# Performance work log

Measured on AMD Instinct MI355X. Metric: run time of the kernel, lower is better.

Reference implementation:

```python
import jax, jax.numpy as jnp
import numpy as np

NUMSTEPS = 10  # message-passing rounds (SeqGGNN numsteps)

def setup_inputs() -> dict:
    key = jax.random.key(0)
    ks = jax.random.split(key, 10)
    B, S, H, V = 64, 512, 256, 32000
    s = 0.05  # keep activations in a stable range
    return {
        "x": jax.random.randint(ks[0], (B, S), 0, V),
        "emb": jax.random.normal(ks[1], (V, H), jnp.float32) * s,
        "W_edge": jax.random.normal(ks[2], (3, H, H), jnp.float32) * s,  # [fwd, bwd, self]
        "b_edge": jax.random.normal(ks[3], (3, H), jnp.float32) * s,
        "W_ih": jax.random.normal(ks[4], (3 * H, H), jnp.float32) * s,
        "W_hh": jax.random.normal(ks[5], (3 * H, H), jnp.float32) * s,
        "b_ih": jax.random.normal(ks[6], (3 * H,), jnp.float32) * s,
        "b_hh": jax.random.normal(ks[7], (3 * H,), jnp.float32) * s,
        "out_w": jax.random.normal(ks[8], (V, H), jnp.float32) * s,
        "out_b": jax.random.normal(ks[9], (V,), jnp.float32) * s,
    }

def _gru(m, h, W_ih, W_hh, b_ih, b_hh):
    # torch.nn.GRUCell semantics with input m, state h
    gi = m @ W_ih.T + b_ih
    gh = h @ W_hh.T + b_hh
    i_r, i_z, i_n = jnp.split(gi, 3, axis=-1)
    h_r, h_z, h_n = jnp.split(gh, 3, axis=-1)
    r = jax.nn.sigmoid(i_r + h_r)
    z = jax.nn.sigmoid(i_z + h_z)
    n = jnp.tanh(i_n + r * h_n)
    return (1.0 - z) * n + z * h

def reference(x, emb, W_edge, b_edge, W_ih, W_hh, b_ih, b_hh, out_w, out_b):
    # x: [B,S] int ids; chain graph per row with 3 edge types:
    #   fwd:  j -> j+1 (node j+1 receives W_edge[0] h_j + b_edge[0])
    #   bwd:  j+1 -> j (node j receives W_edge[1] h_{j+1} + b_edge[1])
    #   self: j -> j   (W_edge[2] h_j + b_edge[2])
    h0 = emb[x]  # [B,S,H]

    def step(h, _):
        t_fwd = jnp.einsum('bsh,hk->bsk', h, W_edge[0]) + b_edge[0]
        t_bwd = jnp.einsum('bsh,hk->bsk', h, W_edge[1]) + b_edge[1]
        m_self = jnp.einsum('bsh,hk->bsk', h, W_edge[2]) + b_edge[2]
        # scatter-sum along the chain == shift with zero pad at boundaries
        m_fwd = jnp.pad(t_fwd[:, :-1], ((0, 0), (1, 0), (0, 0)))
        m_bwd = jnp.pad(t_bwd[:, 1:], ((0, 0), (0, 1), (0, 0)))
        m = m_fwd + m_bwd + m_self
        h_new = _gru(m, h, W_ih, W_hh, b_ih, b_hh)
        return h_new, None

    h, _ = jax.lax.scan(step, h0, None, length=NUMSTEPS)
    last = h[:, -1, :]  # [B,H]
    return last @ out_w.T + out_b  # [B,V]
```

## Files before the change

kernel.cpp:

```cpp
#include <hip/hip_runtime.h>
#include <math.h>

#define Bb 64
#define Ss 512
#define Hh 256
#define Vv 32000
#define BS (Bb*Ss)
#define NSTEPS 10

typedef __attribute__((ext_vector_type(8))) short bf16x8;
typedef __attribute__((ext_vector_type(4))) float f32x4;
typedef unsigned short u16;

#define MFMA(a,b,c) __builtin_amdgcn_mfma_f32_16x16x32_bf16((a),(b),(c),0,0,0)

__device__ __forceinline__ u16 f2bf(float f) {
    unsigned u = __float_as_uint(f);
    u += 0x7fffu + ((u >> 16) & 1u);
    return (u16)(u >> 16);
}
__device__ __forceinline__ float bf2f(u16 h) {
    return __uint_as_float(((unsigned)h) << 16);
}
__device__ __forceinline__ int nmap(int j, int g) {
    return ((j >> 4) << 6) | (g << 4) | (j & 15);
}
#define GLL(src, dst) __builtin_amdgcn_global_load_lds( \
    (const __attribute__((address_space(1))) void*)(src), \
    (__attribute__((address_space(3))) void*)(dst), 16, 0, 0)

__global__ __launch_bounds__(256)
void k_prep_big(const float* __restrict__ We, const float* __restrict__ Wih,
                const float* __restrict__ Whh, u16* __restrict__ Bbig) {
    __shared__ u16 Aps[64 * 32];
    __shared__ u16 Bps[64 * 32];
    const int p = blockIdx.y, seg = p / 3, g = p % 3;
    const int segmap0 = (seg == 0) ? 2 : (seg == 1 ? 0 : 1);
    const float* Wseg = We + segmap0 * 65536;
    const int kt = (blockIdx.x >> 2) * 64, jt = (blockIdx.x & 3) * 64;
    const int t = threadIdx.x;
    const int lane = t & 63, wid = t >> 6;
    const int wy = (wid >> 1) * 32, wx = (wid & 1) * 32;
    const int lr = lane & 15, hi = lane >> 4;

    f32x4 acc[2][2];
    #pragma unroll
    for (int a = 0; a < 2; ++a)
        #pragma unroll
        for (int b = 0; b < 2; ++b) acc[a][b] = 0.0f;

    for (int ks = 0; ks < 8; ++ks) {
        const int k0 = ks * 32;
        {
            int r = t >> 2, kc = t & 3;
            const float* sa = Wseg + (kt + r) * 256 + k0 + kc * 8;
            float4 a0 = *(const float4*)sa, a1 = *(const float4*)(sa + 4);
            bf16x8 va;
            va[0]=(short)f2bf(a0.x); va[1]=(short)f2bf(a0.y); va[2]=(short)f2bf(a0.z); va[3]=(short)f2bf(a0.w);
            va[4]=(short)f2bf(a1.x); va[5]=(short)f2bf(a1.y); va[6]=(short)f2bf(a1.z); va[7]=(short)f2bf(a1.w);
            ((bf16x8*)Aps)[r * 4 + (kc ^ (r & 3))] = va;
            const float* sb = Wih + (g * 256 + jt + r) * 256 + k0 + kc * 8;
            float4 b0 = *(const float4*)sb, b1 = *(const float4*)(sb + 4);
            bf16x8 vb;
            vb[0]=(short)f2bf(b0.x); vb[1]=(short)f2bf(b0.y); vb[2]=(short)f2bf(b0.z); vb[3]=(short)f2bf(b0.w);
            vb[4]=(short)f2bf(b1.x); vb[5]=(short)f2bf(b1.y); vb[6]=(short)f2bf(b1.z); vb[7]=(short)f2bf(b1.w);
            ((bf16x8*)Bps)[r * 4 + (kc ^ (r & 3))] = vb;
        }
        __syncthreads();
        bf16x8 af[2], bfv[2];
        #pragma unroll
        for (int f = 0; f < 2; ++f) {
            int ra = wy + f * 16 + lr;
            af[f]  = ((const bf16x8*)Aps)[ra * 4 + (hi ^ (ra & 3))];
            int rb = wx + f * 16 + lr;
            bfv[f] = ((const bf16x8*)Bps)[rb * 4 + (hi ^ (rb & 3))];
        }
        #pragma unroll
        for (int fm = 0; fm < 2; ++fm)
            #pragma unroll
            for (int fn = 0; fn < 2; ++fn)
                acc[fm][fn] = MFMA(af[fm], bfv[fn], acc[fm][fn]);
        __syncthreads();
    }
    #pragma unroll
    for (int fm = 0; fm < 2; ++fm)
        #pragma unroll
        for (int fn = 0; fn < 2; ++fn) {
            int kbase = kt + wy + fm * 16 + hi * 4;
            int j     = jt + wx + fn * 16 + lr;
            float4 wv = make_float4(0.f, 0.f, 0.f, 0.f);
            if (seg == 0 && g < 2)
                wv = *(const float4*)(Whh + (g * 256 + j) * 256 + kbase);
            ushort4 o;
            o.x = f2bf(acc[fm][fn][0] + wv.x);
            o.y = f2bf(acc[fm][fn][1] + wv.y);
            o.z = f2bf(acc[fm][fn][2] + wv.z);
            o.w = f2bf(acc[fm][fn][3] + wv.w);
            *(ushort4*)(Bbig + (size_t)nmap(j, g) * 768 + seg * 256 + kbase) = o;
        }
}

__global__ __launch_bounds__(256)
void k_prep_hn(const float* __restrict__ Whh, u16* __restrict__ Bbig) {
    int j = blockIdx.x / 3;
    int k = (blockIdx.x % 3) * 256 + threadIdx.x;
    Bbig[(size_t)nmap(j, 3) * 768 + k] =
        (k < 256) ? f2bf(Whh[(512 + j) * 256 + k]) : (u16)0;
}

__global__ __launch_bounds__(256)
void k_prep_bias(const float* __restrict__ Wih, const float* __restrict__ b_edge,
                 const float* __restrict__ b_ih, const float* __restrict__ b_hh,
                 float* __restrict__ bias) {
    int id = blockIdx.x * 256 + threadIdx.x;
    int c = id >> 10, n = id & 1023;
    int g = (n >> 4) & 3;
    int j = ((n >> 6) << 4) | (n & 15);
    float a;
    if (g == 3) {
        a = b_hh[512 + j];
    } else {
        a = b_ih[g * 256 + j] + (g < 2 ? b_hh[g * 256 + j] : 0.f);
        const float* wrow = Wih + (g * 256 + j) * 256;
        for (int k = 0; k < 256; ++k) {
            float eb = b_edge[512 + k] + (c != 0 ? b_edge[k] : 0.f)
                     + (c != 2 ? b_edge[256 + k] : 0.f);
            a += eb * wrow[k];
        }
    }
    bias[c * 1024 + n] = a;
}

__global__ __launch_bounds__(256)
void k_prep_zp(u16* __restrict__ zp) {
    zp[blockIdx.x * 256 + threadIdx.x] = 0;
}

__global__ __launch_bounds__(256)
void k_embed(const int* __restrict__ x, const float* __restrict__ emb,
             u16* __restrict__ h) {
    int idx = blockIdx.x * 256 + threadIdx.x;
    int row = idx >> 5, c8 = idx & 31;
    long long tok = x[row];
    const float4* e = reinterpret_cast<const float4*>(emb + tok * Hh + c8 * 8);
    float4 a = e[0], b = e[1];
    bf16x8 v;
    v[0]=(short)f2bf(a.x); v[1]=(short)f2bf(a.y); v[2]=(short)f2bf(a.z); v[3]=(short)f2bf(a.w);
    v[4]=(short)f2bf(b.x); v[5]=(short)f2bf(b.y); v[6]=(short)f2bf(b.z); v[7]=(short)f2bf(b.w);
    ((bf16x8*)h)[idx] = v;
}

__global__ __launch_bounds__(512, 2)
void k_step(const u16* __restrict__ hin, const u16* __restrict__ Bbig,
            const float* __restrict__ bias, const u16* __restrict__ zp,
            u16* __restrict__ hout) {
    __shared__ __attribute__((aligned(16))) u16 As[2][2][128 * 64];
    __shared__ __attribute__((aligned(16))) u16 Bs[2][2][128 * 64];
    const int t = threadIdx.x;
    const int lane = t & 63, wid = t >> 6;
    const int swz = (blockIdx.x & 7) * 64 + (blockIdx.x >> 3);
    const int rowBlk = (swz >> 2) * 256;
    const int colBlk = (swz & 3) * 256;
    const int wy = wid >> 2, wx = wid & 3;
    const int lr = lane & 15, hi = lane >> 4;
    const int s0 = rowBlk & (Ss - 1);

    const int q   = t >> 3;
    const int off = ((t & 7) ^ (q & 7)) << 3;
    const int xo  = lr & 7;

    const u16* pB[4];
    #pragma unroll
    for (int j = 0; j < 4; ++j)
        pB[j] = Bbig + (size_t)(colBlk + j * 64 + q) * 768 + off;

    f32x4 acc[8][4];
    #pragma unroll
    for (int a = 0; a < 8; ++a)
        #pragma unroll
        for (int b = 0; b < 4; ++b) acc[a][b] = 0.0f;

    #pragma unroll
    for (int h = 0; h < 2; ++h)
        #pragma unroll
        for (int i = 0; i < 2; ++i) {
            int rh = h * 128 + i * 64 + q;
            GLL(hin + (size_t)(rowBlk + rh) * Hh + off,
                &As[0][h][(i * 512 + wid * 64) * 8]);
            GLL(pB[h * 2 + i], &Bs[0][h][(i * 512 + wid * 64) * 8]);
        }
    #pragma unroll
    for (int j = 0; j < 4; ++j) pB[j] += 64;
    __syncthreads();

    #pragma unroll
    for (int seg = 0; seg < 3; ++seg) {
        #pragma unroll
        for (int t4 = 0; t4 < 4; ++t4) {
            const int tt = seg * 4 + t4;
            const int b  = tt & 1, nb = b ^ 1;
            const int tn = tt + 1;
            const int segn = tn >> 2;
            const int dn   = (segn == 0) ? 0 : (segn == 1 ? -1 : 1);
            const int k0n  = (tn & 3) * 64;
            #pragma unroll
            for (int kk = 0; kk < 2; ++kk) {
                bf16x8 bf[4];
                #pragma unroll
                for (int mh = 0; mh < 2; ++mh) {
                    if (tt < 11 && kk == 0) {
                        if (mh == 0) {
                            #pragma unroll
                            for (int h = 0; h < 2; ++h)
                                #pragma unroll
                                for (int i = 0; i < 2; ++i) {
                                    int rh = h * 128 + i * 64 + q;
                                    int ss = s0 + rh + dn;
                                    const u16* src = (ss >= 0 && ss < Ss)
                                        ? hin + (size_t)(rowBlk + rh + dn) * Hh + k0n + off
                                        : zp;
                                    GLL(src, &As[nb][h][(i * 512 + wid * 64) * 8]);
                                }
                        } else {
                            #pragma unroll
                            for (int h = 0; h < 2; ++h)
                                #pragma unroll
                                for (int i = 0; i < 2; ++i)
                                    GLL(pB[h * 2 + i], &Bs[nb][h][(i * 512 + wid * 64) * 8]);
                            #pragma unroll
                            for (int j = 0; j < 4; ++j) pB[j] += 64;
                        }
                    }
                    if (mh == 0) {
                        #pragma unroll
                        for (int f = 0; f < 4; ++f) {
                            if (seg != 0 && f == 3) continue;
                            int rwb = (wx & 1) * 64 + f * 16 + lr;
                            bf[f] = ((const bf16x8*)Bs[b][wx >> 1])
                                        [rwb * 8 + ((kk * 4 + hi) ^ xo)];
                        }
                    }
                    bf16x8 af[4];
                    #pragma unroll
                    for (int f = 0; f < 4; ++f) {
                        int rwa = mh * 64 + f * 16 + lr;
                        af[f] = ((const bf16x8*)As[b][wy])
                                    [rwa * 8 + ((kk * 4 + hi) ^ xo)];
                    }
                    __builtin_amdgcn_s_setprio(1);
                    #pragma unroll
                    for (int fm = 0; fm < 4; ++fm)
                        #pragma unroll
                        for (int fn = 0; fn < 4; ++fn)
                            if (seg == 0 || fn < 3)
                                acc[mh * 4 + fm][fn] =
                                    MFMA(af[fm], bf[fn], acc[mh * 4 + fm][fn]);
                    __builtin_amdgcn_s_setprio(0);
                }
            }
            __syncthreads();
        }
    }

    const int hq = (colBlk >> 2) + wx * 16;
    #pragma unroll
    for (int mf = 0; mf < 8; ++mf)
        #pragma unroll
        for (int i = 0; i < 4; ++i) {
            int row = rowBlk + wy * 128 + mf * 16 + hi * 4 + i;
            int s = row & (Ss - 1);
            int cls = (s == 0) ? 0 : ((s == Ss - 1) ? 2 : 1);
            const float* bp = bias + cls * 1024 + colBlk + wx * 64 + lr;
            float vr = acc[mf][0][i] + bp[0];
            float vz = acc[mf][1][i] + bp[16];
            float vn = acc[mf][2][i] + bp[32];
            float vh = acc[mf][3][i] + bp[48];
            float r = 1.f / (1.f + __expf(-vr));
            float z = 1.f / (1.f + __expf(-vz));
            float e = __expf(2.f * (vn + r * vh));
            float n = 1.f - 2.f / (e + 1.f);
            int hcol = hq + lr;
            float hold = bf2f(hin[(size_t)row * Hh + hcol]);
            hout[(size_t)row * Hh + hcol] = f2bf(n + z * (hold - n));
        }
}

__global__ __launch_bounds__(256)
void k_out(const u16* __restrict__ h, const float* __restrict__ out_w,
           const float* __restrict__ out_b, float* __restrict__ out) {
    __shared__ u16 As[64 * 256];
    const int t = threadIdx.x;
    const int lane = t & 63, wid = t >> 6;
    const int colBlk = blockIdx.x * 128;
    const int wc = wid * 32;
    const int lr = lane & 15, hi = lane >> 4;

    #pragma unroll
    for (int i = 0; i < 8; ++i) {
        int c = t + i * 256;
        int r = c >> 5, kc = c & 31;
        bf16x8 v = *(const bf16x8*)(h + ((size_t)(r * Ss + (Ss - 1))) * Hh + kc * 8);
        ((bf16x8*)As)[r * 32 + (kc ^ (r & 7))] = v;
    }
    __syncthreads();

    f32x4 acc[4][2];
    #pragma unroll
    for (int a = 0; a < 4; ++a) { acc[a][0] = 0.0f; acc[a][1] = 0.0f; }

    #pragma unroll
    for (int ks = 0; ks < 8; ++ks) {
        bf16x8 af[4];
        #pragma unroll
        for (int f = 0; f < 4; ++f) {
            int ra = f * 16 + lr;
            af[f] = ((const bf16x8*)As)[ra * 32 + ((ks * 4 + hi) ^ (ra & 7))];
        }
        #pragma unroll
        for (int fn = 0; fn < 2; ++fn) {
            int n = colBlk + wc + fn * 16 + lr;
            const float* wp = out_w + (size_t)n * 256 + ks * 32 + hi * 8;
            float4 w0 = *(const float4*)wp, w1 = *(const float4*)(wp + 4);
            bf16x8 vb;
            vb[0]=(short)f2bf(w0.x); vb[1]=(short)f2bf(w0.y); vb[2]=(short)f2bf(w0.z); vb[3]=(short)f2bf(w0.w);
            vb[4]=(short)f2bf(w1.x); vb[5]=(short)f2bf(w1.y); vb[6]=(short)f2bf(w1.z); vb[7]=(short)f2bf(w1.w);
            #pragma unroll
            for (int fm = 0; fm < 4; ++fm)
                acc[fm][fn] = MFMA(af[fm], vb, acc[fm][fn]);
        }
    }
    #pragma unroll
    for (int fm = 0; fm < 4; ++fm)
        #pragma unroll
        for (int fn = 0; fn < 2; ++fn)
            #pragma unroll
            for (int i = 0; i < 4; ++i) {
                int row = fm * 16 + hi * 4 + i;
                int col = colBlk + wc + fn * 16 + lr;
                out[(size_t)row * Vv + col] = acc[fm][fn][i] + out_b[col];
            }
}

extern "C" void kernel_launch(void* const* d_in, const int* in_sizes, int n_in,
                              void* d_out, int out_size, void* d_ws, size_t ws_size,
                              hipStream_t stream) {
    const int*   x      = (const int*)  d_in[0];
    const float* emb    = (const float*)d_in[1];
    const float* W_edge = (const float*)d_in[2];
    const float* b_edge = (const float*)d_in[3];
    const float* W_ih   = (const float*)d_in[4];
    const float* W_hh   = (const float*)d_in[5];
    const float* b_ih   = (const float*)d_in[6];
    const float* b_hh   = (const float*)d_in[7];
    const float* out_w  = (const float*)d_in[8];
    const float* out_b  = (const float*)d_in[9];
    float* out = (float*)d_out;

    u16* hA   = (u16*)d_ws;
    u16* hB   = hA + (size_t)BS * Hh;
    u16* Bbig = hB + (size_t)BS * Hh;
    float* bias = (float*)(Bbig + (size_t)1024 * 768);
    u16* zp   = (u16*)(bias + 3 * 1024);

    k_prep_big <<<dim3(16, 9), 256, 0, stream>>>(W_edge, W_ih, W_hh, Bbig);
    k_prep_hn  <<<768, 256, 0, stream>>>(W_hh, Bbig);
    k_prep_bias<<<12, 256, 0, stream>>>(W_ih, b_edge, b_ih, b_hh, bias);
    k_prep_zp  <<<2, 256, 0, stream>>>(zp);
    k_embed    <<<BS * Hh / 8 / 256, 256, 0, stream>>>(x, emb, hA);

    u16* cur = hA;
    u16* nxt = hB;
    for (int step = 0; step < NSTEPS; ++step) {
        k_step<<<512, 512, 0, stream>>>(cur, Bbig, bias, zp, nxt);
        u16* tmp = cur; cur = nxt; nxt = tmp;
    }
    k_out<<<Vv / 128, 256, 0, stream>>>(cur, out_w, out_b, out);
}
```

Measured before the change: 571.2 us.

## Restructure step GEMM main loop into 4-stage K=32 pipeline with fine-grained waits

```diff
diff --git a/kernel.cpp b/kernel.cpp
--- a/kernel.cpp
+++ b/kernel.cpp
@@ -154,8 +154,8 @@
 void k_step(const u16* __restrict__ hin, const u16* __restrict__ Bbig,
             const float* __restrict__ bias, const u16* __restrict__ zp,
             u16* __restrict__ hout) {
-    __shared__ __attribute__((aligned(16))) u16 As[2][2][128 * 64];
-    __shared__ __attribute__((aligned(16))) u16 Bs[2][2][128 * 64];
+    __shared__ __attribute__((aligned(16))) u16 As[4][256 * 32];
+    __shared__ __attribute__((aligned(16))) u16 Bs[4][256 * 32];
     const int t = threadIdx.x;
     const int lane = t & 63, wid = t >> 6;
     const int swz = (blockIdx.x & 7) * 64 + (blockIdx.x >> 3);
@@ -165,14 +165,22 @@
     const int lr = lane & 15, hi = lane >> 4;
     const int s0 = rowBlk & (Ss - 1);
 
-    const int q   = t >> 3;
-    const int off = ((t & 7) ^ (q & 7)) << 3;
-    const int xo  = lr & 7;
-
-    const u16* pB[4];
-    #pragma unroll
-    for (int j = 0; j < 4; ++j)
-        pB[j] = Bbig + (size_t)(colBlk + j * 64 + q) * 768 + off;
+    const int q  = t >> 2;
+    const int kc = t & 3;
+    const u16* baseA[2];
+    const u16* baseB[2];
+    bool edgeLo[2], edgeHi[2];
+    u16* dstOff[2];
+    const u16* zpSafe = zp + 512;
+    #pragma unroll
+    for (int j = 0; j < 2; ++j) {
+        int r  = q + j * 128;
+        int ci = kc ^ (r & 3);
+        baseA[j] = hin  + (size_t)(rowBlk + r) * Hh  + ci * 8;
+        baseB[j] = Bbig + (size_t)(colBlk + r) * 768 + ci * 8;
+        edgeLo[j] = (s0 == 0   && r == 0);
+        edgeHi[j] = (s0 + r == 511);
+    }
 
     f32x4 acc[8][4];
     #pragma unroll
@@ -180,86 +188,61 @@
         #pragma unroll
         for (int b = 0; b < 4; ++b) acc[a][b] = 0.0f;
 
-    #pragma unroll
-    for (int h = 0; h < 2; ++h)
-        #pragma unroll
-        for (int i = 0; i < 2; ++i) {
-            int rh = h * 128 + i * 64 + q;
-            GLL(hin + (size_t)(rowBlk + rh) * Hh + off,
-                &As[0][h][(i * 512 + wid * 64) * 8]);
-            GLL(pB[h * 2 + i], &Bs[0][h][(i * 512 + wid * 64) * 8]);
-        }
-    #pragma unroll
-    for (int j = 0; j < 4; ++j) pB[j] += 64;
-    __syncthreads();
-
-    #pragma unroll
-    for (int seg = 0; seg < 3; ++seg) {
-        #pragma unroll
-        for (int t4 = 0; t4 < 4; ++t4) {
-            const int tt = seg * 4 + t4;
-            const int b  = tt & 1, nb = b ^ 1;
-            const int tn = tt + 1;
-            const int segn = tn >> 2;
-            const int dn   = (segn == 0) ? 0 : (segn == 1 ? -1 : 1);
-            const int k0n  = (tn & 3) * 64;
-            #pragma unroll
-            for (int kk = 0; kk < 2; ++kk) {
-                bf16x8 bf[4];
+    auto STAGE = [&](int tt) {
+        const int seg = tt >> 3;
+        const int d   = (seg == 0) ? 0 : (seg == 1 ? -1 : 1);
+        const int aOff = d * Hh + (tt & 7) * 32;
+        u16* aD = (u16*)As[tt & 3];
+        u16* bD = (u16*)Bs[tt & 3];
+        #pragma unroll
+        for (int j = 0; j < 2; ++j) {
+            const u16* sa = ((d < 0 && edgeLo[j]) || (d > 0 && edgeHi[j]))
+                          ? zpSafe : baseA[j];
+            GLL(sa + aOff,            aD + (size_t)(t + j * 512) * 8);
+            GLL(baseB[j] + tt * 32,   bD + (size_t)(t + j * 512) * 8);
+        }
+    };
+    auto COMPUTE = [&](int tt) {
+        const int seg = tt >> 3;
+        const bf16x8* aB = (const bf16x8*)As[tt & 3];
+        const bf16x8* bB = (const bf16x8*)Bs[tt & 3];
+        bf16x8 bf[4];
+        #pragma unroll
+        for (int f = 0; f < 4; ++f) {
+            if (seg != 0 && f == 3) continue;
+            int rb = wx * 64 + f * 16 + lr;
+            bf[f] = bB[rb * 4 + (hi ^ (rb & 3))];
+        }
+        #pragma unroll
+        for (int mh = 0; mh < 2; ++mh) {
+            bf16x8 af[4];
+            #pragma unroll
+            for (int f = 0; f < 4; ++f) {
+                int ra = wy * 128 + mh * 64 + f * 16 + lr;
+                af[f] = aB[ra * 4 + (hi ^ (ra & 3))];
+            }
+            __builtin_amdgcn_s_setprio(1);
+            #pragma unroll
+            for (int fm = 0; fm < 4; ++fm)
                 #pragma unroll
-                for (int mh = 0; mh < 2; ++mh) {
-                    if (tt < 11 && kk == 0) {
-                        if (mh == 0) {
-                            #pragma unroll
-                            for (int h = 0; h < 2; ++h)
-                                #pragma unroll
-                                for (int i = 0; i < 2; ++i) {
-                                    int rh = h * 128 + i * 64 + q;
-                                    int ss = s0 + rh + dn;
-                                    const u16* src = (ss >= 0 && ss < Ss)
-                                        ? hin + (size_t)(rowBlk + rh + dn) * Hh + k0n + off
-                                        : zp;
-                                    GLL(src, &As[nb][h][(i * 512 + wid * 64) * 8]);
-                                }
-                        } else {
-                            #pragma unroll
-                            for (int h = 0; h < 2; ++h)
-                                #pragma unroll
-                                for (int i = 0; i < 2; ++i)
-                                    GLL(pB[h * 2 + i], &Bs[nb][h][(i * 512 + wid * 64) * 8]);
-                            #pragma unroll
-                            for (int j = 0; j < 4; ++j) pB[j] += 64;
-                        }
-                    }
-                    if (mh == 0) {
-                        #pragma unroll
-                        for (int f = 0; f < 4; ++f) {
-                            if (seg != 0 && f == 3) continue;
-                            int rwb = (wx & 1) * 64 + f * 16 + lr;
-                            bf[f] = ((const bf16x8*)Bs[b][wx >> 1])
-                                        [rwb * 8 + ((kk * 4 + hi) ^ xo)];
-                        }
-                    }
-                    bf16x8 af[4];
-                    #pragma unroll
-                    for (int f = 0; f < 4; ++f) {
-                        int rwa = mh * 64 + f * 16 + lr;
-                        af[f] = ((const bf16x8*)As[b][wy])
-                                    [rwa * 8 + ((kk * 4 + hi) ^ xo)];
-                    }
-                    __builtin_amdgcn_s_setprio(1);
-                    #pragma unroll
-                    for (int fm = 0; fm < 4; ++fm)
-                        #pragma unroll
-                        for (int fn = 0; fn < 4; ++fn)
-                            if (seg == 0 || fn < 3)
-                                acc[mh * 4 + fm][fn] =
-                                    MFMA(af[fm], bf[fn], acc[mh * 4 + fm][fn]);
-                    __builtin_amdgcn_s_setprio(0);
-                }
-            }
-            __syncthreads();
-        }
+                for (int fn = 0; fn < 4; ++fn)
+                    if (seg == 0 || fn < 3)
+                        acc[mh * 4 + fm][fn] = MFMA(af[fm], bf[fn], acc[mh * 4 + fm][fn]);
+            __builtin_amdgcn_s_setprio(0);
+        }
+    };
+
+    STAGE(0);
+    STAGE(1);
+    #pragma unroll
+    for (int tt = 0; tt < 24; ++tt) {
+        if (tt < 22) STAGE(tt + 2);
+        if (tt < 22)       asm volatile("s_waitcnt vmcnt(8)" ::: "memory");
+        else if (tt == 22) asm volatile("s_waitcnt vmcnt(4)" ::: "memory");
+        else               asm volatile("s_waitcnt vmcnt(0)" ::: "memory");
+        __builtin_amdgcn_s_barrier();
+        __builtin_amdgcn_sched_barrier(0);
+        COMPUTE(tt);
     }
 
     const int hq = (colBlk >> 2) + wx * 16;
@@ -365,7 +348,7 @@
     k_prep_big <<<dim3(16, 9), 256, 0, stream>>>(W_edge, W_ih, W_hh, Bbig);
     k_prep_hn  <<<768, 256, 0, stream>>>(W_hh, Bbig);
     k_prep_bias<<<12, 256, 0, stream>>>(W_ih, b_edge, b_ih, b_hh, bias);
-    k_prep_zp  <<<2, 256, 0, stream>>>(zp);
+    k_prep_zp  <<<8, 256, 0, stream>>>(zp);
     k_embed    <<<BS * Hh / 8 / 256, 256, 0, stream>>>(x, emb, hA);
 
     u16* cur = hA;
```

Measured after the change: 604.6 us. +5.8%, slower.

## Restructure k_step main loop into explicit prefetch/compute stages with vmcnt waits

Applied to the files above, without the earlier changes.

```diff
diff --git a/kernel.cpp b/kernel.cpp
--- a/kernel.cpp
+++ b/kernel.cpp
@@ -180,86 +180,73 @@
         #pragma unroll
         for (int b = 0; b < 4; ++b) acc[a][b] = 0.0f;
 
-    #pragma unroll
-    for (int h = 0; h < 2; ++h)
-        #pragma unroll
-        for (int i = 0; i < 2; ++i) {
-            int rh = h * 128 + i * 64 + q;
-            GLL(hin + (size_t)(rowBlk + rh) * Hh + off,
-                &As[0][h][(i * 512 + wid * 64) * 8]);
-            GLL(pB[h * 2 + i], &Bs[0][h][(i * 512 + wid * 64) * 8]);
-        }
-    #pragma unroll
-    for (int j = 0; j < 4; ++j) pB[j] += 64;
-    __syncthreads();
-
-    #pragma unroll
-    for (int seg = 0; seg < 3; ++seg) {
-        #pragma unroll
-        for (int t4 = 0; t4 < 4; ++t4) {
-            const int tt = seg * 4 + t4;
-            const int b  = tt & 1, nb = b ^ 1;
-            const int tn = tt + 1;
-            const int segn = tn >> 2;
-            const int dn   = (segn == 0) ? 0 : (segn == 1 ? -1 : 1);
-            const int k0n  = (tn & 3) * 64;
-            #pragma unroll
-            for (int kk = 0; kk < 2; ++kk) {
-                bf16x8 bf[4];
+    auto STAGE = [&](int tt) {
+        const int buf = tt & 1;
+        const int seg = tt >> 2;
+        const int d   = (seg == 0) ? 0 : (seg == 1 ? -1 : 1);
+        const int k0  = (tt & 3) * 64;
+        #pragma unroll
+        for (int h = 0; h < 2; ++h)
+            #pragma unroll
+            for (int i = 0; i < 2; ++i) {
+                int rh = h * 128 + i * 64 + q;
+                int ss = s0 + rh + d;
+                const u16* sa = (ss >= 0 && ss < Ss)
+                    ? hin + (size_t)(rowBlk + rh + d) * Hh + k0 + off
+                    : zp;
+                GLL(sa, &As[buf][h][(i * 512 + wid * 64) * 8]);
+                GLL(pB[h * 2 + i] + tt * 64, &Bs[buf][h][(i * 512 + wid * 64) * 8]);
+            }
+    };
+    auto COMPUTE = [&](int tt) {
+        const int buf = tt & 1;
+        const int seg = tt >> 2;
+        #pragma unroll
+        for (int kk = 0; kk < 2; ++kk) {
+            bf16x8 bfv[4];
+            #pragma unroll
+            for (int f = 0; f < 4; ++f) {
+                if (seg != 0 && f == 3) continue;
+                int rwb = (wx & 1) * 64 + f * 16 + lr;
+                bfv[f] = ((const bf16x8*)Bs[buf][wx >> 1])
+                            [rwb * 8 + ((kk * 4 + hi) ^ xo)];
+            }
+            #pragma unroll
+            for (int mh = 0; mh < 2; ++mh) {
+                bf16x8 af[4];
                 #pragma unroll
-                for (int mh = 0; mh < 2; ++mh) {
-                    if (tt < 11 && kk == 0) {
-                        if (mh == 0) {
-                            #pragma unroll
-                            for (int h = 0; h < 2; ++h)
-                                #pragma unroll
-                                for (int i = 0; i < 2; ++i) {
-                                    int rh = h * 128 + i * 64 + q;
-                                    int ss = s0 + rh + dn;
-                                    const u16* src = (ss >= 0 && ss < Ss)
-                                        ? hin + (size_t)(rowBlk + rh + dn) * Hh + k0n + off
-                                        : zp;
-                                    GLL(src, &As[nb][h][(i * 512 + wid * 64) * 8]);
-                                }
-                        } else {
-                            #pragma unroll
-                            for (int h = 0; h < 2; ++h)
-                                #pragma unroll
-                                for (int i = 0; i < 2; ++i)
-                                    GLL(pB[h * 2 + i], &Bs[nb][h][(i * 512 + wid * 64) * 8]);
-                            #pragma unroll
-                            for (int j = 0; j < 4; ++j) pB[j] += 64;
-                        }
-                    }
-                    if (mh == 0) {
-                        #pragma unroll
-                        for (int f = 0; f < 4; ++f) {
-                            if (seg != 0 && f == 3) continue;
-                            int rwb = (wx & 1) * 64 + f * 16 + lr;
-                            bf[f] = ((const bf16x8*)Bs[b][wx >> 1])
-                                        [rwb * 8 + ((kk * 4 + hi) ^ xo)];
-                        }
-                    }
-                    bf16x8 af[4];
+                for (int f = 0; f < 4; ++f) {
+                    int rwa = mh * 64 + f * 16 + lr;
+                    af[f] = ((const bf16x8*)As[buf][wy])
+                                [rwa * 8 + ((kk * 4 + hi) ^ xo)];
+                }
+                __builtin_amdgcn_s_setprio(1);
+                #pragma unroll
+                for (int fm = 0; fm < 4; ++fm)
                     #pragma unroll
-                    for (int f = 0; f < 4; ++f) {
-                        int rwa = mh * 64 + f * 16 + lr;
-                        af[f] = ((const bf16x8*)As[b][wy])
-                                    [rwa * 8 + ((kk * 4 + hi) ^ xo)];
-                    }
-                    __builtin_amdgcn_s_setprio(1);
-                    #pragma unroll
-                    for (int fm = 0; fm < 4; ++fm)
-                        #pragma unroll
-                        for (int fn = 0; fn < 4; ++fn)
-                            if (seg == 0 || fn < 3)
-                                acc[mh * 4 + fm][fn] =
-                                    MFMA(af[fm], bf[fn], acc[mh * 4 + fm][fn]);
-                    __builtin_amdgcn_s_setprio(0);
-                }
+                    for (int fn = 0; fn < 4; ++fn)
+                        if (seg == 0 || fn < 3)
+                            acc[mh * 4 + fm][fn] =
+                                MFMA(af[fm], bfv[fn], acc[mh * 4 + fm][fn]);
+                __builtin_amdgcn_s_setprio(0);
             }
-            __syncthreads();
-        }
+        }
+    };
+
+    STAGE(0);
+    #pragma unroll
+    for (int tt = 0; tt < 12; ++tt) {
+        if (tt < 11) {
+            STAGE(tt + 1);
+            asm volatile("s_waitcnt vmcnt(8)" ::: "memory");
+        } else {
+            asm volatile("s_waitcnt vmcnt(0)" ::: "memory");
+        }
+        __builtin_amdgcn_s_barrier();
+        __builtin_amdgcn_sched_barrier(0);
+        COMPUTE(tt);
+        __builtin_amdgcn_s_barrier();
+        __builtin_amdgcn_sched_barrier(0);
     }
 
     const int hq = (colBlk >> 2) + wx * 16;
@@ -365,7 +352,7 @@
     k_prep_big <<<dim3(16, 9), 256, 0, stream>>>(W_edge, W_ih, W_hh, Bbig);
     k_prep_hn  <<<768, 256, 0, stream>>>(W_hh, Bbig);
     k_prep_bias<<<12, 256, 0, stream>>>(W_ih, b_edge, b_ih, b_hh, bias);
-    k_prep_zp  <<<2, 256, 0, stream>>>(zp);
+    k_prep_zp  <<<8, 256, 0, stream>>>(zp);
     k_embed    <<<BS * Hh / 8 / 256, 256, 0, stream>>>(x, emb, hA);
 
     u16* cur = hA;
```

Measured after the change: 598.5 us (median of 4 runs). 4.8% more time.
